# Kernel tuning notes

Hardware: AMD Instinct MI355X
Metric: run time of the kernel (lower is better)

## Reference

```python
import math
import jax, jax.numpy as jnp
from jax import lax
import numpy as np

B = 4
WIN = 2048          # t == win_len
N_EMBD = 512
N_HEAD = 8
SUB_LEN = 64
QLEN = 1
HEAD_DIM = N_EMBD // N_HEAD          # v head dim
SCALE = HEAD_DIM ** -0.5             # scale=True uses head_dim, not q/k width


def _row_mask(index, sub_len, win_len):
    mask = np.zeros(win_len, dtype=np.float32)
    log_l = math.ceil(math.log2(sub_len))
    if (win_len // sub_len) * 2 * log_l > index:
        mask[: index + 1] = 1
    else:
        i = index
        while i >= 0:
            start = i - log_l + 1
            if start < 0:
                mask[:i] = 1
                break
            mask[start : i + 1] = 1
            for j in range(log_l):
                ni = start - 2 ** j
                if ni >= 0 and i - ni <= sub_len:
                    mask[ni] = 1
            i -= sub_len
    return mask


def _log_mask(win_len, sub_len):
    m = np.zeros((win_len, win_len), dtype=np.float32)
    for i in range(win_len):
        m[i] = _row_mask(i, sub_len, win_len)
    return m


def setup_inputs() -> dict:
    key = jax.random.key(0)
    k0, k1, k2, k3 = jax.random.split(key, 4)
    x = jax.random.normal(k0, (B, WIN, N_EMBD), jnp.float32)
    # Conv1d weight: [out_channels=2*h*e, in_channels=e, kernel=q_len]
    w_qk = jax.random.normal(k1, (N_EMBD * N_HEAD * 2, N_EMBD, QLEN), jnp.float32) * 0.02
    w_v = jax.random.normal(k2, (N_EMBD, N_EMBD), jnp.float32) * 0.02
    b_v = jnp.zeros((N_EMBD,), jnp.float32)
    w_proj = jax.random.normal(k3, (N_EMBD, N_EMBD), jnp.float32) * 0.02
    b_proj = jnp.zeros((N_EMBD,), jnp.float32)
    mask = jnp.asarray(_log_mask(WIN, SUB_LEN) > 0)
    return {"x": x, "w_qk": w_qk, "w_v": w_v, "b_v": b_v,
            "w_proj": w_proj, "b_proj": b_proj, "mask": mask}


def reference(x, w_qk, w_v, b_v, w_proj, b_proj, mask):
    b, t, e = x.shape
    # value: pointwise linear -> [b, h, t, head_dim]
    v = (x @ w_v + b_v).reshape(b, t, N_HEAD, HEAD_DIM).transpose(0, 2, 1, 3)
    # query_key: causal conv1d with left padding (q_len - 1)
    qk = lax.conv_general_dilated(
        x.transpose(0, 2, 1), w_qk, (1,), [(QLEN - 1, 0)],
        dimension_numbers=("NCH", "OIH", "NCH"))  # [b, 2*h*e, t]
    qk = qk.transpose(0, 2, 1)                    # [b, t, 2*h*e]
    q, k = jnp.split(qk, 2, axis=-1)              # each [b, t, h*e]
    q = q.reshape(b, t, N_HEAD, e).transpose(0, 2, 1, 3)  # [b, h, t, e]
    k = k.reshape(b, t, N_HEAD, e).transpose(0, 2, 1, 3)  # [b, h, t, e]
    scores = jnp.einsum("bhqe,bhke->bhqk", q, k) * SCALE   # [b, h, t, t]
    scores = jnp.where(mask[:t, :t], scores, -jnp.inf)
    attn = jax.nn.softmax(scores, axis=-1)
    ctx = jnp.einsum("bhqk,bhkd->bhqd", attn, v)           # [b, h, t, hd]
    ctx = ctx.transpose(0, 2, 1, 3).reshape(b, t, -1)      # [b, t, e]
    return ctx @ w_proj + b_proj
```

## Files before the change

kernel.cpp:

```cpp
#include <hip/hip_runtime.h>
#include <stdint.h>


typedef __attribute__((ext_vector_type(8))) short short8;
typedef __attribute__((ext_vector_type(4))) float f32x4;
typedef __attribute__((ext_vector_type(4))) unsigned short us4;

__device__ __forceinline__ f32x4 fzero4() { f32x4 z = {0.f, 0.f, 0.f, 0.f}; return z; }

__device__ __forceinline__ unsigned short f2bf(float f) {
  unsigned u = __float_as_uint(f);
  u += 0x7fff + ((u >> 16) & 1);
  return (unsigned short)(u >> 16);
}

__device__ __forceinline__ void gload_lds16(const void* g, void* l) {
  __builtin_amdgcn_global_load_lds((const __attribute__((address_space(1))) void*)g,
                                   (__attribute__((address_space(3))) void*)l, 16, 0, 0);
}

__device__ __forceinline__ int xcd_swizzle(int flat, int nwg) {
  const int cpx = nwg >> 3;
  return (flat & 7) * cpx + (flat >> 3);
}

template <int EPI>
__global__ __launch_bounds__(256, 2) void gemm_bt(const unsigned short* __restrict__ A,
                                                  const unsigned short* __restrict__ B,
                                                  void* __restrict__ Cout,
                                                  const float* __restrict__ bias,
                                                  int M, int N, int K) {
  __shared__ unsigned short As[128 * 32];
  __shared__ unsigned short Bs[128 * 32];
  const int tid = threadIdx.x;
  const int wid = tid >> 6;
  const int lane = tid & 63;
  const int wm = wid >> 1, wn = wid & 1;
  const int nbx = (M + 127) / 128;
  const int sw = xcd_swizzle(blockIdx.y * gridDim.x + blockIdx.x, gridDim.x * gridDim.y);
  const long m0 = (long)(sw % nbx) * 128;
  const long n0 = (long)(sw / nbx) * 128;

  f32x4 acc[4][4];
#pragma unroll
  for (int i = 0; i < 4; ++i)
#pragma unroll
    for (int j = 0; j < 4; ++j) acc[i][j] = fzero4();

  const int lrow = tid >> 2;
  const int lcol = (tid & 3) * 8;
  const unsigned short* Ag = A + (m0 + lrow) * (long)K + lcol;
  const unsigned short* Bg = B + (n0 + lrow) * (long)K + lcol;
  unsigned short* Asl = As + tid * 8;
  unsigned short* Bsl = Bs + tid * 8;
  const long K64 = (long)64 * K;

  const int fr = lane & 15;
  const int fk = (lane >> 4) * 8;

  for (int k0 = 0; k0 < K; k0 += 32) {
    gload_lds16(Ag + k0, Asl);
    gload_lds16(Ag + K64 + k0, Asl + 2048);
    gload_lds16(Bg + k0, Bsl);
    gload_lds16(Bg + K64 + k0, Bsl + 2048);
    __syncthreads();
    short8 af[4], bfr[4];
#pragma unroll
    for (int i = 0; i < 4; ++i) af[i] = *(const short8*)&As[(wm * 64 + i * 16 + fr) * 32 + fk];
#pragma unroll
    for (int j = 0; j < 4; ++j) bfr[j] = *(const short8*)&Bs[(wn * 64 + j * 16 + fr) * 32 + fk];
#pragma unroll
    for (int i = 0; i < 4; ++i)
#pragma unroll
      for (int j = 0; j < 4; ++j)
        acc[i][j] = __builtin_amdgcn_mfma_f32_16x16x32_bf16(af[i], bfr[j], acc[i][j], 0, 0, 0);
    __syncthreads();
  }

  const int fg = lane >> 4;
#pragma unroll
  for (int i = 0; i < 4; ++i) {
#pragma unroll
    for (int j = 0; j < 4; ++j) {
      const long row0 = m0 + wm * 64 + i * 16 + fg * 4;
      const long col = n0 + wn * 64 + j * 16 + fr;
      if (EPI == 0) {
        unsigned short* C = (unsigned short*)Cout;
#pragma unroll
        for (int r = 0; r < 4; ++r) C[(row0 + r) * (long)N + col] = f2bf(acc[i][j][r]);
      } else if (EPI == 1) {
        unsigned short* C = (unsigned short*)Cout;
        const float bs = bias[col];
        const int b_ = (int)(row0 >> 11);
        const int t0 = (int)(row0 & 2047);
        us4 pk;
#pragma unroll
        for (int r = 0; r < 4; ++r) pk[r] = f2bf(acc[i][j][r] + bs);
        *(us4*)&C[((size_t)(b_ * 512 + col)) * 2048 + t0] = pk;
      } else {
        float* C = (float*)Cout;
        const float bs = bias[col];
#pragma unroll
        for (int r = 0; r < 4; ++r) C[(row0 + r) * (long)N + col] = acc[i][j][r] + bs;
      }
    }
  }
}

#define STAGE(BUF, G)                                                          \
  do {                                                                         \
    const int _kt = (G) >> 1, _hf = (G) & 1;                                   \
    const unsigned short* _src = Kg + (size_t)(_kt) * (64 * 8192) + _hf * 256; \
    _Pragma("unroll") for (int _r = 0; _r < 8; ++_r)                           \
        gload_lds16(_src + (size_t)_r * 8 * 8192, &Kb[BUF][_r * 2048 + tid * 8]); \
  } while (0)

#define QK_HALF(BUF, HF)                                                       \
  __builtin_amdgcn_s_setprio(1);                                               \
  _Pragma("unroll") for (int e8 = 0; e8 < 8; ++e8) {                           \
    _Pragma("unroll") for (int j = 0; j < 2; ++j) {                            \
      const int _row = wn * 32 + j * 16 + fr;                                  \
      const short8 bfr = *(const short8*)&Kb[BUF][_row * 256 +                 \
                                                  (((e8 * 4 + fg) ^ xsw) << 3)]; \
      s[0][j] = __builtin_amdgcn_mfma_f32_16x16x32_bf16(qreg[0][(HF)*8 + e8],  \
                                                        bfr, s[0][j], 0, 0, 0); \
      s[1][j] = __builtin_amdgcn_mfma_f32_16x16x32_bf16(qreg[1][(HF)*8 + e8],  \
                                                        bfr, s[1][j], 0, 0, 0); \
    }                                                                          \
  }                                                                            \
  __builtin_amdgcn_s_setprio(0);

__global__ __launch_bounds__(256, 2) void flash_attn(const unsigned short* __restrict__ QK,
                                                     const unsigned short* __restrict__ Vt,
                                                     unsigned short* __restrict__ ctx) {
  __shared__ unsigned short Kb[2][64 * 256];
  __shared__ unsigned short Plds[4][32 * 32];

  const int tid = threadIdx.x, wid = tid >> 6, lane = tid & 63;
  const int fr = lane & 15, fg = lane >> 4;
  const int xsw = fr & 7;
  const int wm = wid >> 1, wn = wid & 1;

  const int id = blockIdx.x;
  const int bh = (id & 7) * 4 + ((id >> 3) & 3);
  const int p = id >> 5;
  const int b = bh >> 3, h = bh & 7;

  const int gslot = (tid & 31) ^ (tid >> 5);
  const unsigned short* Kg =
      QK + (size_t)(b * 2048 + (tid >> 5)) * 8192 + 4096 + h * 512 + gslot * 8;

  short8 ones;
#pragma unroll
  for (int z = 0; z < 8; ++z) ones[z] = (short)0x3F80;

  float* Osc = (float*)&Kb[0][0];
  float* lsc = (float*)&Kb[1][0];

  for (int tile = 0; tile < 2; ++tile) {
    const int qt = (tile == 0) ? (31 - p) : p;

    short8 qreg[2][16];
    {
      const unsigned short* qp =
          QK + (size_t)(b * 2048 + qt * 64 + wm * 32 + fr) * 8192 + h * 512 + fg * 8;
#pragma unroll
      for (int i = 0; i < 2; ++i)
#pragma unroll
        for (int e = 0; e < 16; ++e)
          qreg[i][e] = *(const short8*)(qp + (size_t)i * 16 * 8192 + e * 32);
    }

    unsigned m_gen[2], m_t0[2], m_diag[2];
#pragma unroll
    for (int i = 0; i < 2; ++i) {
      const int lrow = wm * 32 + i * 16 + fg * 4;
      m_gen[i] = 0xFFu; m_t0[i] = 0xFFu; m_diag[i] = 0u;
      if (qt <= 5) {
#pragma unroll
        for (int r = 0; r < 4; ++r)
#pragma unroll
          for (int j = 0; j < 2; ++j)
            if (wn * 32 + j * 16 + fr <= lrow + r) m_diag[i] |= 1u << (r * 2 + j);
      } else {
        m_gen[i] = 0; m_t0[i] = 0;
        const unsigned long long SBITS = 0x20002022FFull;
#pragma unroll
        for (int r = 0; r < 4; ++r) {
          const int irow = qt * 64 + lrow + r;
#pragma unroll
          for (int j = 0; j < 2; ++j) {
            const int c = wn * 32 + j * 16 + fr;
            const int t = (irow - c) & 63;
            const unsigned g = (unsigned)((SBITS >> t) & 1ull);
            const unsigned bit = 1u << (r * 2 + j);
            if (g) m_gen[i] |= bit;
            if ((c + t >= 5) ? (g != 0) : (t >= 1)) m_t0[i] |= bit;
            if (g && c <= lrow + r) m_diag[i] |= bit;
          }
        }
      }
    }

    f32x4 o[2][4], ol[2];
#pragma unroll
    for (int i = 0; i < 2; ++i) {
      ol[i] = fzero4();
#pragma unroll
      for (int j = 0; j < 4; ++j) o[i][j] = fzero4();
    }

    STAGE(0, 0);

    for (int kt = 0; kt <= qt; ++kt) {
      f32x4 s[2][2];
#pragma unroll
      for (int i = 0; i < 2; ++i)
#pragma unroll
        for (int j = 0; j < 2; ++j) s[i][j] = fzero4();

      __syncthreads();
      STAGE(1, kt * 2 + 1);
      QK_HALF(0, 0);

      __syncthreads();
      if (kt < qt) STAGE(0, (kt + 1) * 2);
      short8 vreg[4];
#pragma unroll
      for (int jd = 0; jd < 4; ++jd)
        vreg[jd] = *(const short8*)(Vt + (size_t)(bh * 64 + jd * 16 + fr) * 2048 +
                                    kt * 64 + wn * 32 + fg * 8);
      QK_HALF(1, 1);

#pragma unroll
      for (int i = 0; i < 2; ++i) {
        unsigned mm = (kt == 0) ? m_t0[i] : m_gen[i];
        if (kt == qt) mm &= m_diag[i];
#pragma unroll
        for (int r = 0; r < 4; ++r) {
#pragma unroll
          for (int j = 0; j < 2; ++j) {
            float v = s[i][j][r] * 0.18033688f;
            v = ((mm >> (r * 2 + j)) & 1u) ? v : -1e30f;
            const float pv = __builtin_amdgcn_exp2f(v);
            const int prow = i * 16 + fg * 4 + r;
            Plds[wid][prow * 32 + ((((j << 1) + (fr >> 3)) ^ r) << 3) + (fr & 7)] =
                f2bf(pv);
          }
        }
      }

      __builtin_amdgcn_s_setprio(1);
#pragma unroll
      for (int i = 0; i < 2; ++i) {
        const int arow = i * 16 + fr;
        const short8 pa = *(const short8*)&Plds[wid][arow * 32 + ((fg ^ (fr & 3)) << 3)];
#pragma unroll
        for (int jd = 0; jd < 4; ++jd)
          o[i][jd] = __builtin_amdgcn_mfma_f32_16x16x32_bf16(pa, vreg[jd], o[i][jd], 0, 0, 0);
        ol[i] = __builtin_amdgcn_mfma_f32_16x16x32_bf16(pa, ones, ol[i], 0, 0, 0);
      }
      __builtin_amdgcn_s_setprio(0);
    }

    __syncthreads();
    if (wn == 1) {
#pragma unroll
      for (int i = 0; i < 2; ++i) {
#pragma unroll
        for (int r = 0; r < 4; ++r) {
          const int row32 = wm * 32 + i * 16 + fg * 4 + r;
#pragma unroll
          for (int jd = 0; jd < 4; ++jd)
            Osc[row32 * 64 + jd * 16 + fr] = o[i][jd][r];
          if (fr == 0) lsc[row32] = ol[i][r];
        }
      }
    }
    __syncthreads();
    if (wn == 0) {
#pragma unroll
      for (int i = 0; i < 2; ++i) {
#pragma unroll
        for (int r = 0; r < 4; ++r) {
          const int row32 = wm * 32 + i * 16 + fg * 4 + r;
          const float l = ol[i][r] + lsc[row32];
          const float inv = 1.0f / l;
          unsigned short* cp =
              ctx + (size_t)(b * 2048 + qt * 64 + row32) * 512 + h * 64;
#pragma unroll
          for (int jd = 0; jd < 4; ++jd) {
            const float v = o[i][jd][r] + Osc[row32 * 64 + jd * 16 + fr];
            cp[jd * 16 + fr] = f2bf(v * inv);
          }
        }
      }
    }
    __syncthreads();
  }
}

__global__ void f32_to_bf16_k(const float* __restrict__ in, unsigned short* __restrict__ out,
                              int n4) {
  const int i = blockIdx.x * 256 + threadIdx.x;
  if (i < n4) {
    const float4 v = ((const float4*)in)[i];
    us4 o;
    o[0] = f2bf(v.x);
    o[1] = f2bf(v.y);
    o[2] = f2bf(v.z);
    o[3] = f2bf(v.w);
    ((us4*)out)[i] = o;
  }
}

__global__ void transpose_w_k(const float* __restrict__ in, unsigned short* __restrict__ out) {
  const int idx = blockIdx.x * 256 + threadIdx.x;
  const int row = idx >> 9, col = idx & 511;
  out[idx] = f2bf(in[col * 512 + row]);
}

extern "C" void kernel_launch(void* const* d_in, const int* in_sizes, int n_in,
                              void* d_out, int out_size, void* d_ws, size_t ws_size,
                              hipStream_t stream) {
  (void)in_sizes; (void)n_in; (void)out_size; (void)ws_size;
  const float* x = (const float*)d_in[0];
  const float* wqk = (const float*)d_in[1];
  const float* wv = (const float*)d_in[2];
  const float* bv = (const float*)d_in[3];
  const float* wp = (const float*)d_in[4];
  const float* bp = (const float*)d_in[5];

  char* ws = (char*)d_ws;
  unsigned short* x_bf   = (unsigned short*)(ws + 0);
  unsigned short* wqk_bf = (unsigned short*)(ws + (size_t)8 * 1048576);
  unsigned short* wv_t   = (unsigned short*)(ws + (size_t)16 * 1048576);
  unsigned short* wp_t   = (unsigned short*)(ws + (size_t)17 * 1048576);
  unsigned short* qk_bf  = (unsigned short*)(ws + (size_t)18 * 1048576);
  unsigned short* v_t    = (unsigned short*)(ws + (size_t)146 * 1048576);
  unsigned short* ctx_bf = (unsigned short*)(ws + (size_t)154 * 1048576);

  f32_to_bf16_k<<<4096, 256, 0, stream>>>(x, x_bf, 1048576);
  f32_to_bf16_k<<<4096, 256, 0, stream>>>(wqk, wqk_bf, 1048576);
  transpose_w_k<<<1024, 256, 0, stream>>>(wv, wv_t);
  transpose_w_k<<<1024, 256, 0, stream>>>(wp, wp_t);

  gemm_bt<0><<<dim3(64, 64), 256, 0, stream>>>(x_bf, wqk_bf, qk_bf, nullptr, 8192, 8192, 512);
  gemm_bt<1><<<dim3(64, 4), 256, 0, stream>>>(x_bf, wv_t, v_t, bv, 8192, 512, 512);

  flash_attn<<<512, 256, 0, stream>>>(qk_bf, v_t, ctx_bf);

  gemm_bt<2><<<dim3(64, 4), 256, 0, stream>>>(ctx_bf, wp_t, d_out, bp, 8192, 512, 512);
}
```

Baseline: 286.3 us.

## Stage K in quarter chunks to shrink LDS and allow three blocks per CU

```diff
diff --git a/kernel.cpp b/kernel.cpp
--- a/kernel.cpp
+++ b/kernel.cpp
@@ -107,34 +107,34 @@
   }
 }
 
-#define STAGE(BUF, G)                                                          \
-  do {                                                                         \
-    const int _kt = (G) >> 1, _hf = (G) & 1;                                   \
-    const unsigned short* _src = Kg + (size_t)(_kt) * (64 * 8192) + _hf * 256; \
-    _Pragma("unroll") for (int _r = 0; _r < 8; ++_r)                           \
-        gload_lds16(_src + (size_t)_r * 8 * 8192, &Kb[BUF][_r * 2048 + tid * 8]); \
+#define STAGE(BUF, G)                                                           \
+  do {                                                                          \
+    const unsigned short* _src =                                                \
+        Kg + (size_t)((G) >> 2) * (64 * 8192) + ((G) & 3) * 128;                \
+    _Pragma("unroll") for (int _r = 0; _r < 4; ++_r)                            \
+        gload_lds16(_src + (size_t)_r * 16 * 8192, &Kb[BUF][_r * 2048 + tid * 8]); \
   } while (0)
 
-#define QK_HALF(BUF, HF)                                                       \
-  __builtin_amdgcn_s_setprio(1);                                               \
-  _Pragma("unroll") for (int e8 = 0; e8 < 8; ++e8) {                           \
-    _Pragma("unroll") for (int j = 0; j < 2; ++j) {                            \
-      const int _row = wn * 32 + j * 16 + fr;                                  \
-      const short8 bfr = *(const short8*)&Kb[BUF][_row * 256 +                 \
-                                                  (((e8 * 4 + fg) ^ xsw) << 3)]; \
-      s[0][j] = __builtin_amdgcn_mfma_f32_16x16x32_bf16(qreg[0][(HF)*8 + e8],  \
+#define QK_QTR(BUF, C)                                                          \
+  __builtin_amdgcn_s_setprio(1);                                                \
+  _Pragma("unroll") for (int e = 0; e < 4; ++e) {                               \
+    _Pragma("unroll") for (int j = 0; j < 2; ++j) {                             \
+      const int _row = wn * 32 + j * 16 + fr;                                   \
+      const short8 bfr = *(const short8*)&Kb[BUF][_row * 128 +                  \
+                                                  (((e * 4 + fg) ^ xsw) << 3)]; \
+      s[0][j] = __builtin_amdgcn_mfma_f32_16x16x32_bf16(qreg[0][(C) * 4 + e],   \
                                                         bfr, s[0][j], 0, 0, 0); \
-      s[1][j] = __builtin_amdgcn_mfma_f32_16x16x32_bf16(qreg[1][(HF)*8 + e8],  \
+      s[1][j] = __builtin_amdgcn_mfma_f32_16x16x32_bf16(qreg[1][(C) * 4 + e],   \
                                                         bfr, s[1][j], 0, 0, 0); \
-    }                                                                          \
-  }                                                                            \
+    }                                                                           \
+  }                                                                             \
   __builtin_amdgcn_s_setprio(0);
 
-__global__ __launch_bounds__(256, 2) void flash_attn(const unsigned short* __restrict__ QK,
+__global__ __launch_bounds__(256, 3) void flash_attn(const unsigned short* __restrict__ QK,
                                                      const unsigned short* __restrict__ Vt,
                                                      unsigned short* __restrict__ ctx) {
-  __shared__ unsigned short Kb[2][64 * 256];
-  __shared__ unsigned short Plds[4][32 * 32];
+  __shared__ unsigned short Kb[2][64 * 128];
+  __shared__ unsigned short Plds[4][16 * 40];
 
   const int tid = threadIdx.x, wid = tid >> 6, lane = tid & 63;
   const int fr = lane & 15, fg = lane >> 4;
@@ -146,9 +146,9 @@
   const int p = id >> 5;
   const int b = bh >> 3, h = bh & 7;
 
-  const int gslot = (tid & 31) ^ (tid >> 5);
+  const int gslot = (tid & 15) ^ ((tid >> 4) & 7);
   const unsigned short* Kg =
-      QK + (size_t)(b * 2048 + (tid >> 5)) * 8192 + 4096 + h * 512 + gslot * 8;
+      QK + (size_t)(b * 2048 + (tid >> 4)) * 8192 + 4096 + h * 512 + gslot * 8;
 
   short8 ones;
 #pragma unroll
@@ -159,6 +159,7 @@
 
   for (int tile = 0; tile < 2; ++tile) {
     const int qt = (tile == 0) ? (31 - p) : p;
+    const int NG = (qt + 1) * 4;
 
     short8 qreg[2][16];
     {
@@ -210,6 +211,7 @@
       for (int j = 0; j < 4; ++j) o[i][j] = fzero4();
     }
 
+    int cur = 0;
     STAGE(0, 0);
 
     for (int kt = 0; kt <= qt; ++kt) {
@@ -218,19 +220,22 @@
       for (int i = 0; i < 2; ++i)
 #pragma unroll
         for (int j = 0; j < 2; ++j) s[i][j] = fzero4();
-
-      __syncthreads();
-      STAGE(1, kt * 2 + 1);
-      QK_HALF(0, 0);
-
-      __syncthreads();
-      if (kt < qt) STAGE(0, (kt + 1) * 2);
       short8 vreg[4];
-#pragma unroll
-      for (int jd = 0; jd < 4; ++jd)
-        vreg[jd] = *(const short8*)(Vt + (size_t)(bh * 64 + jd * 16 + fr) * 2048 +
-                                    kt * 64 + wn * 32 + fg * 8);
-      QK_HALF(1, 1);
+
+#pragma unroll
+      for (int c = 0; c < 4; ++c) {
+        __syncthreads();
+        const int g = kt * 4 + c;
+        if (g + 1 < NG) STAGE(cur ^ 1, g + 1);
+        if (c == 2) {
+#pragma unroll
+          for (int jd = 0; jd < 4; ++jd)
+            vreg[jd] = *(const short8*)(Vt + (size_t)(bh * 64 + jd * 16 + fr) * 2048 +
+                                        kt * 64 + wn * 32 + fg * 8);
+        }
+        QK_QTR(cur, c);
+        cur ^= 1;
+      }
 
 #pragma unroll
       for (int i = 0; i < 2; ++i) {
@@ -243,24 +248,17 @@
             float v = s[i][j][r] * 0.18033688f;
             v = ((mm >> (r * 2 + j)) & 1u) ? v : -1e30f;
             const float pv = __builtin_amdgcn_exp2f(v);
-            const int prow = i * 16 + fg * 4 + r;
-            Plds[wid][prow * 32 + ((((j << 1) + (fr >> 3)) ^ r) << 3) + (fr & 7)] =
-                f2bf(pv);
+            Plds[wid][(fg * 4 + r) * 40 + j * 16 + fr] = f2bf(pv);
           }
         }
-      }
-
-      __builtin_amdgcn_s_setprio(1);
-#pragma unroll
-      for (int i = 0; i < 2; ++i) {
-        const int arow = i * 16 + fr;
-        const short8 pa = *(const short8*)&Plds[wid][arow * 32 + ((fg ^ (fr & 3)) << 3)];
+        __builtin_amdgcn_s_setprio(1);
+        const short8 pa = *(const short8*)&Plds[wid][fr * 40 + fg * 8];
 #pragma unroll
         for (int jd = 0; jd < 4; ++jd)
           o[i][jd] = __builtin_amdgcn_mfma_f32_16x16x32_bf16(pa, vreg[jd], o[i][jd], 0, 0, 0);
         ol[i] = __builtin_amdgcn_mfma_f32_16x16x32_bf16(pa, ones, ol[i], 0, 0, 0);
-      }
-      __builtin_amdgcn_s_setprio(0);
+        __builtin_amdgcn_s_setprio(0);
+      }
     }
 
     __syncthreads();
```

Result: slower. 565.5 us (+97.5%).

## Replace QK projection GEMM with 256x256-tile double-buffered swizzled-LDS kernel

Applied to the files above, without the earlier changes.

```diff
diff --git a/kernel.cpp b/kernel.cpp
--- a/kernel.cpp
+++ b/kernel.cpp
@@ -22,6 +22,93 @@
 __device__ __forceinline__ int xcd_swizzle(int flat, int nwg) {
   const int cpx = nwg >> 3;
   return (flat & 7) * cpx + (flat >> 3);
+}
+
+#define STAGE256(D, KT)                                                            \
+  do {                                                                             \
+    _Pragma("unroll") for (int l = 0; l < 4; ++l) {                                \
+      gload_lds16(Ab + (size_t)l * 32768 + (KT) * 64, &S[D][0][l * 4096 + tid * 8]); \
+      gload_lds16(Bb + (size_t)l * 32768 + (KT) * 64, &S[D][1][l * 4096 + tid * 8]); \
+    }                                                                              \
+  } while (0)
+
+__global__ __launch_bounds__(512, 2) void gemm256(const unsigned short* __restrict__ A,
+                                                  const unsigned short* __restrict__ B,
+                                                  unsigned short* __restrict__ C) {
+  __shared__ unsigned short S[2][2][16384];
+
+  const int tid = threadIdx.x;
+  const int wid = tid >> 6, lane = tid & 63;
+  const int fr = lane & 15, fg = lane >> 4;
+  const int wm = wid >> 2, wn = wid & 3;
+
+  const int sw = xcd_swizzle(blockIdx.x, 1024);
+  const long m0 = (long)(sw & 31) * 256;
+  const long n0 = (long)(sw >> 5) * 256;
+
+  const int gslot = (tid & 7) ^ ((tid >> 3) & 7);
+  const unsigned short* Ab = A + (m0 + (tid >> 3)) * 512 + gslot * 8;
+  const unsigned short* Bb = B + (n0 + (tid >> 3)) * 512 + gslot * 8;
+
+  f32x4 acc[8][4];
+#pragma unroll
+  for (int i = 0; i < 8; ++i)
+#pragma unroll
+    for (int j = 0; j < 4; ++j) acc[i][j] = fzero4();
+
+  STAGE256(0, 0);
+
+  const int xsw = fr & 7;
+  for (int kt = 0; kt < 8; ++kt) {
+    const int d = kt & 1;
+    if (kt < 7) {
+      STAGE256(d ^ 1, kt + 1);
+      asm volatile("s_waitcnt vmcnt(8)" ::: "memory");
+    } else {
+      asm volatile("s_waitcnt vmcnt(0)" ::: "memory");
+    }
+    __builtin_amdgcn_s_barrier();
+
+    short8 bfr[4][2];
+#pragma unroll
+    for (int nf = 0; nf < 4; ++nf)
+#pragma unroll
+      for (int ks = 0; ks < 2; ++ks)
+        bfr[nf][ks] = *(const short8*)&S[d][1][(wn * 64 + nf * 16 + fr) * 64 +
+                                               (((ks * 4 + fg) ^ xsw) << 3)];
+#pragma unroll
+    for (int mh = 0; mh < 2; ++mh) {
+      short8 af[4][2];
+#pragma unroll
+      for (int mf = 0; mf < 4; ++mf)
+#pragma unroll
+        for (int ks = 0; ks < 2; ++ks)
+          af[mf][ks] = *(const short8*)&S[d][0][(wm * 128 + mh * 64 + mf * 16 + fr) * 64 +
+                                                (((ks * 4 + fg) ^ xsw) << 3)];
+      __builtin_amdgcn_s_setprio(1);
+#pragma unroll
+      for (int mf = 0; mf < 4; ++mf)
+#pragma unroll
+        for (int nf = 0; nf < 4; ++nf)
+#pragma unroll
+          for (int ks = 0; ks < 2; ++ks)
+            acc[mh * 4 + mf][nf] = __builtin_amdgcn_mfma_f32_16x16x32_bf16(
+                af[mf][ks], bfr[nf][ks], acc[mh * 4 + mf][nf], 0, 0, 0);
+      __builtin_amdgcn_s_setprio(0);
+    }
+    __builtin_amdgcn_s_barrier();
+  }
+
+#pragma unroll
+  for (int mf = 0; mf < 8; ++mf) {
+#pragma unroll
+    for (int nf = 0; nf < 4; ++nf) {
+      const long row0 = m0 + wm * 128 + mf * 16 + fg * 4;
+      const long col = n0 + wn * 64 + nf * 16 + fr;
+#pragma unroll
+      for (int r = 0; r < 4; ++r) C[(row0 + r) * 8192 + col] = f2bf(acc[mf][nf][r]);
+    }
+  }
 }
 
 template <int EPI>
@@ -84,11 +171,7 @@
     for (int j = 0; j < 4; ++j) {
       const long row0 = m0 + wm * 64 + i * 16 + fg * 4;
       const long col = n0 + wn * 64 + j * 16 + fr;
-      if (EPI == 0) {
-        unsigned short* C = (unsigned short*)Cout;
-#pragma unroll
-        for (int r = 0; r < 4; ++r) C[(row0 + r) * (long)N + col] = f2bf(acc[i][j][r]);
-      } else if (EPI == 1) {
+      if (EPI == 1) {
         unsigned short* C = (unsigned short*)Cout;
         const float bs = bias[col];
         const int b_ = (int)(row0 >> 11);
@@ -345,7 +428,7 @@
   transpose_w_k<<<1024, 256, 0, stream>>>(wv, wv_t);
   transpose_w_k<<<1024, 256, 0, stream>>>(wp, wp_t);
 
-  gemm_bt<0><<<dim3(64, 64), 256, 0, stream>>>(x_bf, wqk_bf, qk_bf, nullptr, 8192, 8192, 512);
+  gemm256<<<1024, 512, 0, stream>>>(x_bf, wqk_bf, qk_bf);
   gemm_bt<1><<<dim3(64, 4), 256, 0, stream>>>(x_bf, wv_t, v_t, bv, 8192, 512, 512);
 
   flash_attn<<<512, 256, 0, stream>>>(qk_bf, v_t, ctx_bf);
```

New measurement: 275.1 us. 1.04x faster.
